# Optimization experiments

Hardware: AMD Instinct MI355X
Metric: run time of the kernel (lower is better)

The kernel has to match this reference:

```python
import jax, jax.numpy as jnp
import numpy as np
from jax import lax

NUM_MARKETS = 32
WINDOW = 16
T = 1048576


def setup_inputs() -> dict:
    key = jax.random.key(0)
    k1, k2, k3, k4 = jax.random.split(key, 4)
    std = float(np.sqrt(WINDOW))  # matches nn.init.normal_(.., 0, sqrt(window_size))
    x = jax.random.normal(k1, (1, NUM_MARKETS, T), dtype=jnp.float32)
    start_pos = -jnp.ones((NUM_MARKETS, 1), dtype=jnp.float32)  # default start_pos = -1
    conv_w = jax.random.normal(k2, (NUM_MARKETS, NUM_MARKETS, WINDOW), dtype=jnp.float32) * std
    conv_b = jax.random.normal(k3, (NUM_MARKETS,), dtype=jnp.float32) * 0.05
    pos_weight = jax.random.normal(k4, (NUM_MARKETS, 1), dtype=jnp.float32) * std
    return {"x": x, "start_pos": start_pos, "conv_w": conv_w, "conv_b": conv_b, "pos_weight": pos_weight}


def reference(x, start_pos, conv_w, conv_b, pos_weight):
    # Conv1d, valid padding: [1, N, T] -> [1, N, L], L = T - WINDOW + 1
    y = lax.conv_general_dilated(
        x, conv_w, window_strides=(1,), padding="VALID",
        dimension_numbers=("NCH", "OIH", "NCH"),
    ) + conv_b[None, :, None]
    seq = y[0].T  # [L, N] time-major for the scan
    pw = pos_weight[:, 0]  # [N]

    def step(pos, xt):
        a = jnp.tanh(pos * pw + xt)  # [N]
        return jnp.sign(a), a

    _, outs = lax.scan(step, start_pos[:, 0], seq)  # outs: [L, N]
    positions = jnp.concatenate([start_pos, outs.T], axis=1)  # [N, L+1]
    return positions[None]  # [1, N, L+1]
```

## Files before the change

### kernel.cpp

```cpp
#include <hip/hip_runtime.h>
#include <stdint.h>

#define T_LEN    1048576
#define TY_LEN   1048561
#define OUT_W    1048562
#define NM       32
#define WIN      16
#define NCH32    32768
#define CBT      256
#define TPB      256
#define XS_W     272
#define NF4      68

__device__ inline float sgnf(float a){
    return (a > 0.0f) ? 1.0f : ((a < 0.0f) ? -1.0f : 0.0f);
}

__device__ inline uint32_t map_comp(uint32_t f, uint32_t g){
    uint32_t r = 0;
#pragma unroll
    for (int k = 0; k < 4; ++k) {
        const uint32_t s = (g >> (8 * k)) & 0xFFu;
        const uint32_t o = (f >> (8 * s)) & 0xFFu;
        r |= o << (8 * k);
    }
    return r;
}

__global__ void wtrans_kernel(const float* __restrict__ w, float* __restrict__ wT2){
    const int idx = blockIdx.x * 256 + threadIdx.x;
    if (idx >= NM * NM * WIN) return;
    const int o = idx / (NM * WIN);
    const int r = idx - o * (NM * WIN);
    const int i = r / WIN;
    const int h = r - i * WIN;
    wT2[(((h * 4) + (o >> 3)) * NM + i) * 8 + (o & 7)] = w[idx];
}

__global__ __launch_bounds__(256, 4) void conv_kernel(
    const float* __restrict__ x, const float* __restrict__ wT2,
    const float* __restrict__ b, const float* __restrict__ sp,
    const float* __restrict__ pwv, float* __restrict__ out,
    uint32_t* __restrict__ trans)
{
    __shared__ float xs[NM * XS_W];
    const int base = blockIdx.x * TPB;
    for (int idx = threadIdx.x; idx < NM * NF4; idx += CBT) {
        const int i = idx / NF4;
        const int q = idx - i * NF4;
        const int t0 = base + q * 4;
        float4 v;
        if (t0 + 3 < T_LEN) {
            v = *reinterpret_cast<const float4*>(x + (size_t)i * T_LEN + t0);
        } else {
            v.x = (t0 + 0 < T_LEN) ? x[(size_t)i * T_LEN + t0 + 0] : 0.0f;
            v.y = (t0 + 1 < T_LEN) ? x[(size_t)i * T_LEN + t0 + 1] : 0.0f;
            v.z = (t0 + 2 < T_LEN) ? x[(size_t)i * T_LEN + t0 + 2] : 0.0f;
            v.w = (t0 + 3 < T_LEN) ? x[(size_t)i * T_LEN + t0 + 3] : 0.0f;
        }
        *reinterpret_cast<float4*>(&xs[i * XS_W + q * 4]) = v;
    }
    __syncthreads();
    const int lane = threadIdx.x & 63;
    const int og   = __builtin_amdgcn_readfirstlane(threadIdx.x >> 6);
    float acc[8][4];
#pragma unroll
    for (int oi = 0; oi < 8; ++oi)
#pragma unroll
        for (int tt = 0; tt < 4; ++tt) acc[oi][tt] = 0.0f;
#pragma unroll 1
    for (int h = 0; h < WIN; ++h) {
        const float* wp = wT2 + (size_t)(h * 4 + og) * (NM * 8);
#pragma unroll 1
        for (int c = 0; c < 4; ++c) {
            float xv[8][4];
#pragma unroll
            for (int i2 = 0; i2 < 8; ++i2) {
                const int i = c * 8 + i2;
#pragma unroll
                for (int tt = 0; tt < 4; ++tt)
                    xv[i2][tt] = xs[i * XS_W + lane + 64 * tt + h];
            }
#pragma unroll
            for (int i2 = 0; i2 < 8; ++i2) {
                const float* wr = wp + (c * 8 + i2) * 8;
#pragma unroll
                for (int oi = 0; oi < 8; ++oi) {
                    const float wv = wr[oi];
#pragma unroll
                    for (int tt = 0; tt < 4; ++tt)
                        acc[oi][tt] = fmaf(wv, xv[i2][tt], acc[oi][tt]);
                }
            }
        }
    }
    float yv[8][4];
    __syncthreads();
#pragma unroll
    for (int oi = 0; oi < 8; ++oi) {
        const int o = og * 8 + oi;
        const float bv = b[o];
#pragma unroll
        for (int tt = 0; tt < 4; ++tt) {
            yv[oi][tt] = acc[oi][tt] + bv;
            const int sub = (lane >> 5) + 2 * tt;
            xs[(o * 8 + sub) * 33 + (lane & 31)] = yv[oi][tt];
        }
    }
    __syncthreads();
#pragma unroll
    for (int oi = 0; oi < 8; ++oi) {
        const int o = og * 8 + oi;
        float* orow = out + (size_t)o * OUT_W + 1 + base + lane;
#pragma unroll
        for (int tt = 0; tt < 4; ++tt) {
            const int t = base + lane + 64 * tt;
            if (t < TY_LEN) orow[64 * tt] = yv[oi][tt];
        }
    }
    {
        const int sm = threadIdx.x >> 3;
        const int ss = threadIdx.x & 7;
        const float pws = pwv[sm];
        float q0 = -1.0f, q1 = 0.0f, q2 = 1.0f, q3 = sp[sm];
        int st = TY_LEN - base - ss * 32;
        st = st < 0 ? 0 : (st > 32 ? 32 : st);
        const float* yr = &xs[(sm * 8 + ss) * 33];
        for (int j = 0; j < st; ++j) {
            const float hv = yr[j];
            q0 = sgnf(fmaf(q0, pws, hv));
            q1 = sgnf(fmaf(q1, pws, hv));
            q2 = sgnf(fmaf(q2, pws, hv));
            q3 = sgnf(fmaf(q3, pws, hv));
        }
        const uint32_t e0 = (uint32_t)((int)q0 + 1);
        const uint32_t e1 = (uint32_t)((int)q1 + 1);
        const uint32_t e2 = (uint32_t)((int)q2 + 1);
        const uint32_t e3 = (st == 0) ? 3u : (uint32_t)((int)q3 + 1);
        trans[(size_t)sm * NCH32 + blockIdx.x * 8 + ss] =
            e0 | (e1 << 8) | (e2 << 16) | (e3 << 24);
    }
}

__global__ __launch_bounds__(256) void scan_pass_b(
    const uint32_t* __restrict__ trans, uint8_t* __restrict__ entries)
{
    const uint32_t ID = 0x03020100u;
    const int m = blockIdx.x;
    const int tid = threadIdx.x;
    __shared__ uint32_t S[256];
    const uint32_t* tr = trans + (size_t)m * NCH32 + tid * 128;
    uint32_t seg = ID;
    for (int j = 0; j < 128; ++j) seg = map_comp(tr[j], seg);
    S[tid] = seg;
    __syncthreads();
    for (int off = 1; off < 256; off <<= 1) {
        const uint32_t v = (tid >= off) ? S[tid - off] : ID;
        __syncthreads();
        if (tid >= off) S[tid] = map_comp(S[tid], v);
        __syncthreads();
    }
    const uint32_t pre = (tid == 0) ? ID : S[tid - 1];
    uint32_t s = (pre >> 24) & 0xFFu;
    uint8_t* er = entries + (size_t)m * NCH32 + tid * 128;
    for (int j = 0; j < 128; ++j) {
        er[j] = (uint8_t)s;
        s = (tr[j] >> (8 * s)) & 0xFFu;
    }
}

__global__ __launch_bounds__(256) void scan_pass_c(
    float* yo, const float* __restrict__ sp, const float* __restrict__ pwv,
    const uint8_t* __restrict__ entries)
{
    const int gid = blockIdx.x * 256 + threadIdx.x;
    const int m = gid >> 15;
    const int c = gid & (NCH32 - 1);
    const float pw = pwv[m];
    const float spv = sp[m];
    const uint32_t s = entries[(size_t)m * NCH32 + c];
    float p = (s == 3u) ? spv : ((float)(int)s - 1.0f);
    float* row = yo + (size_t)m * OUT_W + 1 + (size_t)c * 32;
    if (c == 0) yo[(size_t)m * OUT_W] = spv;
    const int limit0 = TY_LEN - c * 32;
    const int limit = limit0 < 32 ? limit0 : 32;
    if (limit == 32) {
#pragma unroll
        for (int j = 0; j < 32; j += 4) {
            const float4 h = *reinterpret_cast<const float4*>(row + j);
            float a;
            a = fmaf(p, pw, h.x); row[j+0] = tanhf(a); p = sgnf(a);
            a = fmaf(p, pw, h.y); row[j+1] = tanhf(a); p = sgnf(a);
            a = fmaf(p, pw, h.z); row[j+2] = tanhf(a); p = sgnf(a);
            a = fmaf(p, pw, h.w); row[j+3] = tanhf(a); p = sgnf(a);
        }
    } else {
        for (int j = 0; j < limit; ++j) {
            const float a = fmaf(p, pw, row[j]);
            row[j] = tanhf(a);
            p = sgnf(a);
        }
    }
}

extern "C" void kernel_launch(void* const* d_in, const int* in_sizes, int n_in,
                              void* d_out, int out_size, void* d_ws, size_t ws_size,
                              hipStream_t stream)
{
    const float* x   = (const float*)d_in[0];
    const float* spv = (const float*)d_in[1];
    const float* w   = (const float*)d_in[2];
    const float* b   = (const float*)d_in[3];
    const float* pw  = (const float*)d_in[4];
    float* out = (float*)d_out;

    uint8_t* ws = (uint8_t*)d_ws;
    float*    wT2     = (float*)ws;
    uint32_t* trans   = (uint32_t*)(ws + 65536);
    uint8_t*  entries = (uint8_t*)(ws + 65536 + (size_t)NM * NCH32 * 4);

    wtrans_kernel<<<64, 256, 0, stream>>>(w, wT2);
    conv_kernel<<<4096, CBT, 0, stream>>>(x, wT2, b, spv, pw, out, trans);
    scan_pass_b<<<NM, 256, 0, stream>>>(trans, entries);
    scan_pass_c<<<(NM * NCH32) / 256, 256, 0, stream>>>(out, spv, pw, entries);
}
```

Measured before the change: 529.8 us.

## Fuse chunk scan into conv kernel with decoupled lookback across blocks

```diff
diff --git a/kernel.cpp b/kernel.cpp
--- a/kernel.cpp
+++ b/kernel.cpp
@@ -6,25 +6,34 @@
 #define OUT_W    1048562
 #define NM       32
 #define WIN      16
-#define NCH32    32768
+#define NBLK     4096
 #define CBT      256
 #define TPB      256
 #define XS_W     272
 #define NF4      68
+#define ID8      0xE4u
 
 __device__ inline float sgnf(float a){
     return (a > 0.0f) ? 1.0f : ((a < 0.0f) ? -1.0f : 0.0f);
 }
 
-__device__ inline uint32_t map_comp(uint32_t f, uint32_t g){
+__device__ inline uint32_t comp2(uint32_t f, uint32_t g){
     uint32_t r = 0;
 #pragma unroll
     for (int k = 0; k < 4; ++k) {
-        const uint32_t s = (g >> (8 * k)) & 0xFFu;
-        const uint32_t o = (f >> (8 * s)) & 0xFFu;
-        r |= o << (8 * k);
+        const uint32_t s = (g >> (2 * k)) & 3u;
+        r |= ((f >> (2 * s)) & 3u) << (2 * k);
     }
     return r;
+}
+
+__device__ inline uint32_t agg_load(const uint32_t* p){
+    uint32_t w = __hip_atomic_load(p, __ATOMIC_RELAXED, __HIP_MEMORY_SCOPE_AGENT);
+    while (!(w & 0x80000000u)) {
+        __builtin_amdgcn_s_sleep(2);
+        w = __hip_atomic_load(p, __ATOMIC_RELAXED, __HIP_MEMORY_SCOPE_AGENT);
+    }
+    return w;
 }
 
 __global__ void wtrans_kernel(const float* __restrict__ w, float* __restrict__ wT2){
@@ -41,10 +50,14 @@
     const float* __restrict__ x, const float* __restrict__ wT2,
     const float* __restrict__ b, const float* __restrict__ sp,
     const float* __restrict__ pwv, float* __restrict__ out,
-    uint32_t* __restrict__ trans)
+    uint32_t* __restrict__ agg)
 {
     __shared__ float xs[NM * XS_W];
-    const int base = blockIdx.x * TPB;
+    __shared__ uint32_t maps8[256];
+    __shared__ uint32_t parts[256];
+    __shared__ uint32_t entryS[NM];
+    const int bid  = blockIdx.x;
+    const int base = bid * TPB;
     for (int idx = threadIdx.x; idx < NM * NF4; idx += CBT) {
         const int i = idx / NF4;
         const int q = idx - i * NF4;
@@ -94,7 +107,6 @@
             }
         }
     }
-    float yv[8][4];
     __syncthreads();
 #pragma unroll
     for (int oi = 0; oi < 8; ++oi) {
@@ -102,29 +114,19 @@
         const float bv = b[o];
 #pragma unroll
         for (int tt = 0; tt < 4; ++tt) {
-            yv[oi][tt] = acc[oi][tt] + bv;
             const int sub = (lane >> 5) + 2 * tt;
-            xs[(o * 8 + sub) * 33 + (lane & 31)] = yv[oi][tt];
-        }
-    }
-    __syncthreads();
-#pragma unroll
-    for (int oi = 0; oi < 8; ++oi) {
-        const int o = og * 8 + oi;
-        float* orow = out + (size_t)o * OUT_W + 1 + base + lane;
-#pragma unroll
-        for (int tt = 0; tt < 4; ++tt) {
-            const int t = base + lane + 64 * tt;
-            if (t < TY_LEN) orow[64 * tt] = yv[oi][tt];
-        }
-    }
+            xs[(o * 8 + sub) * 33 + (lane & 31)] = acc[oi][tt] + bv;
+        }
+    }
+    __syncthreads();
+    const int sm = threadIdx.x >> 3;
+    const int ss = threadIdx.x & 7;
+    const float pws = pwv[sm];
+    const float spv = sp[sm];
+    int st = TY_LEN - base - ss * 32;
+    st = st < 0 ? 0 : (st > 32 ? 32 : st);
     {
-        const int sm = threadIdx.x >> 3;
-        const int ss = threadIdx.x & 7;
-        const float pws = pwv[sm];
-        float q0 = -1.0f, q1 = 0.0f, q2 = 1.0f, q3 = sp[sm];
-        int st = TY_LEN - base - ss * 32;
-        st = st < 0 ? 0 : (st > 32 ? 32 : st);
+        float q0 = -1.0f, q1 = 0.0f, q2 = 1.0f, q3 = spv;
         const float* yr = &xs[(sm * 8 + ss) * 33];
         for (int j = 0; j < st; ++j) {
             const float hv = yr[j];
@@ -137,70 +139,77 @@
         const uint32_t e1 = (uint32_t)((int)q1 + 1);
         const uint32_t e2 = (uint32_t)((int)q2 + 1);
         const uint32_t e3 = (st == 0) ? 3u : (uint32_t)((int)q3 + 1);
-        trans[(size_t)sm * NCH32 + blockIdx.x * 8 + ss] =
-            e0 | (e1 << 8) | (e2 << 16) | (e3 << 24);
-    }
-}
-
-__global__ __launch_bounds__(256) void scan_pass_b(
-    const uint32_t* __restrict__ trans, uint8_t* __restrict__ entries)
-{
-    const uint32_t ID = 0x03020100u;
-    const int m = blockIdx.x;
-    const int tid = threadIdx.x;
-    __shared__ uint32_t S[256];
-    const uint32_t* tr = trans + (size_t)m * NCH32 + tid * 128;
-    uint32_t seg = ID;
-    for (int j = 0; j < 128; ++j) seg = map_comp(tr[j], seg);
-    S[tid] = seg;
-    __syncthreads();
-    for (int off = 1; off < 256; off <<= 1) {
-        const uint32_t v = (tid >= off) ? S[tid - off] : ID;
-        __syncthreads();
-        if (tid >= off) S[tid] = map_comp(S[tid], v);
-        __syncthreads();
-    }
-    const uint32_t pre = (tid == 0) ? ID : S[tid - 1];
-    uint32_t s = (pre >> 24) & 0xFFu;
-    uint8_t* er = entries + (size_t)m * NCH32 + tid * 128;
-    for (int j = 0; j < 128; ++j) {
-        er[j] = (uint8_t)s;
-        s = (tr[j] >> (8 * s)) & 0xFFu;
-    }
-}
-
-__global__ __launch_bounds__(256) void scan_pass_c(
-    float* yo, const float* __restrict__ sp, const float* __restrict__ pwv,
-    const uint8_t* __restrict__ entries)
-{
-    const int gid = blockIdx.x * 256 + threadIdx.x;
-    const int m = gid >> 15;
-    const int c = gid & (NCH32 - 1);
-    const float pw = pwv[m];
-    const float spv = sp[m];
-    const uint32_t s = entries[(size_t)m * NCH32 + c];
-    float p = (s == 3u) ? spv : ((float)(int)s - 1.0f);
-    float* row = yo + (size_t)m * OUT_W + 1 + (size_t)c * 32;
-    if (c == 0) yo[(size_t)m * OUT_W] = spv;
-    const int limit0 = TY_LEN - c * 32;
-    const int limit = limit0 < 32 ? limit0 : 32;
-    if (limit == 32) {
-#pragma unroll
-        for (int j = 0; j < 32; j += 4) {
-            const float4 h = *reinterpret_cast<const float4*>(row + j);
-            float a;
-            a = fmaf(p, pw, h.x); row[j+0] = tanhf(a); p = sgnf(a);
-            a = fmaf(p, pw, h.y); row[j+1] = tanhf(a); p = sgnf(a);
-            a = fmaf(p, pw, h.z); row[j+2] = tanhf(a); p = sgnf(a);
-            a = fmaf(p, pw, h.w); row[j+3] = tanhf(a); p = sgnf(a);
-        }
-    } else {
-        for (int j = 0; j < limit; ++j) {
-            const float a = fmaf(p, pw, row[j]);
-            row[j] = tanhf(a);
+        maps8[threadIdx.x] = e0 | (e1 << 2) | (e2 << 4) | (e3 << 6);
+    }
+    __syncthreads();
+    if (threadIdx.x < NM) {
+        uint32_t seg = ID8;
+#pragma unroll
+        for (int s2 = 0; s2 < 8; ++s2) seg = comp2(maps8[threadIdx.x * 8 + s2], seg);
+        __hip_atomic_store(&agg[(size_t)threadIdx.x * NBLK + bid],
+                           0x80000000u | seg,
+                           __ATOMIC_RELAXED, __HIP_MEMORY_SCOPE_AGENT);
+    }
+    {
+        uint32_t part = ID8;
+        const int q = (bid + 7) >> 3;
+        int lo = ss * q;
+        int hi = lo + q; if (hi > bid) hi = bid;
+        const uint32_t* ar = agg + (size_t)sm * NBLK;
+        int j = lo;
+        for (; j + 8 <= hi; j += 8) {
+            uint32_t wb[8];
+#pragma unroll
+            for (int u = 0; u < 8; ++u)
+                wb[u] = __hip_atomic_load(&ar[j + u], __ATOMIC_RELAXED,
+                                          __HIP_MEMORY_SCOPE_AGENT);
+#pragma unroll
+            for (int u = 0; u < 8; ++u) {
+                uint32_t w = wb[u];
+                while (!(w & 0x80000000u)) {
+                    __builtin_amdgcn_s_sleep(2);
+                    w = __hip_atomic_load(&ar[j + u], __ATOMIC_RELAXED,
+                                          __HIP_MEMORY_SCOPE_AGENT);
+                }
+                part = comp2(w, part);
+            }
+        }
+        for (; j < hi; ++j) part = comp2(agg_load(&ar[j]), part);
+        parts[threadIdx.x] = part;
+    }
+    __syncthreads();
+    if (threadIdx.x < NM) {
+        uint32_t pre = ID8;
+#pragma unroll
+        for (int k = 0; k < 8; ++k) pre = comp2(parts[threadIdx.x * 8 + k], pre);
+        entryS[threadIdx.x] = (pre >> 6) & 3u;
+    }
+    __syncthreads();
+    {
+        uint32_t s = entryS[sm];
+        for (int k = 0; k < ss; ++k) s = (maps8[sm * 8 + k] >> (2 * s)) & 3u;
+        float p = (s == 3u) ? spv : ((float)(int)s - 1.0f);
+        float* yr = &xs[(sm * 8 + ss) * 33];
+        for (int j = 0; j < st; ++j) {
+            const float a = fmaf(p, pws, yr[j]);
+            yr[j] = tanhf(a);
             p = sgnf(a);
         }
     }
+    __syncthreads();
+#pragma unroll
+    for (int oi = 0; oi < 8; ++oi) {
+        const int o = og * 8 + oi;
+        float* orow = out + (size_t)o * OUT_W + 1 + base + lane;
+#pragma unroll
+        for (int tt = 0; tt < 4; ++tt) {
+            const int t = base + lane + 64 * tt;
+            const int sub = (lane >> 5) + 2 * tt;
+            if (t < TY_LEN) orow[64 * tt] = xs[(o * 8 + sub) * 33 + (lane & 31)];
+        }
+    }
+    if (bid == 0 && threadIdx.x < NM)
+        out[(size_t)threadIdx.x * OUT_W] = sp[threadIdx.x];
 }
 
 extern "C" void kernel_launch(void* const* d_in, const int* in_sizes, int n_in,
@@ -215,12 +224,10 @@
     float* out = (float*)d_out;
 
     uint8_t* ws = (uint8_t*)d_ws;
-    float*    wT2     = (float*)ws;
-    uint32_t* trans   = (uint32_t*)(ws + 65536);
-    uint8_t*  entries = (uint8_t*)(ws + 65536 + (size_t)NM * NCH32 * 4);
-
+    float*    wT2 = (float*)ws;
+    uint32_t* agg = (uint32_t*)(ws + 65536);
+
+    hipMemsetAsync(agg, 0, (size_t)NM * NBLK * 4, stream);
     wtrans_kernel<<<64, 256, 0, stream>>>(w, wT2);
-    conv_kernel<<<4096, CBT, 0, stream>>>(x, wT2, b, spv, pw, out, trans);
-    scan_pass_b<<<NM, 256, 0, stream>>>(trans, entries);
-    scan_pass_c<<<(NM * NCH32) / 256, 256, 0, stream>>>(out, spv, pw, entries);
-}
+    conv_kernel<<<NBLK, CBT, 0, stream>>>(x, wT2, b, spv, pw, out, agg);
+}
```

After: 1.168 ms. 120% more time.
